# Optimization experiments

Measured on AMD Instinct MI355X. Metric: run time of the kernel, lower is better.

Reference implementation:

```python
import jax, jax.numpy as jnp
import numpy as np

B, S, E, H, A = 2, 1024, 1024, 16, 3
HD = E // H

def setup_inputs() -> dict:
    key = jax.random.key(0)
    ks = jax.random.split(key, 8)
    return {
        "query": jax.random.normal(ks[0], (B, S, E), dtype=jnp.float32),
        "key": jax.random.normal(ks[1], (B, S, E), dtype=jnp.float32),
        "value": jax.random.normal(ks[2], (B, S, E), dtype=jnp.float32),
        "aid": jax.random.normal(ks[3], (B, S, S, A), dtype=jnp.float32),
        "mixer_w": jax.random.uniform(ks[4], (H, A + 1, 1), dtype=jnp.float32),
        "mixer_b": jax.random.uniform(ks[5], (H, 1), dtype=jnp.float32),
        "Wo": jax.random.normal(ks[6], (E, E), dtype=jnp.float32) * 0.02,
        "bo": jax.random.normal(ks[7], (E,), dtype=jnp.float32) * 0.02,
        "aid_scale": jnp.array([0.1], dtype=jnp.float32),
    }

def reference(query, key, value, aid, mixer_w, mixer_b, Wo, bo, aid_scale):
    scale = HD ** -0.5
    # Faithful to source: raw row-major reshape (B,S,E)->(B,H,S,HD)
    q = query.reshape(B, H, S, HD)
    k = key.reshape(B, H, S, HD)
    v = value.reshape(B, H, S, HD)
    attn = jnp.einsum('bhqd,bhkd->bhqk', q, k) * scale  # (B,H,S,S)
    aid_h = jnp.broadcast_to(aid[:, None], (B, H, S, S, A))
    mix_in = jnp.concatenate([attn[..., None], aid_h], axis=-1)  # (B,H,S,S,A+1)
    mixed = jnp.einsum('bhqki,hio->bhqko', mix_in, mixer_w) + mixer_b[None, :, None, None, :]
    mixed = jax.nn.relu(mixed)[..., 0]  # (B,H,S,S)
    attn = attn + mixed * aid_scale[0]
    pre_softmax_attn = attn
    attn = jax.nn.softmax(attn, axis=-1)
    out = jnp.einsum('bhqk,bhkd->bhqd', attn, v)
    out = out.transpose(0, 2, 1, 3).reshape(B, S, E)
    out = out @ Wo.T + bo
    return out, attn, pre_softmax_attn
```

## Files before the change

### kernel.cpp

```cpp
#include <hip/hip_runtime.h>
#include <hip/hip_bf16.h>

using u16 = unsigned short;
typedef __attribute__((ext_vector_type(8))) short short8;
typedef __attribute__((ext_vector_type(4))) float f32x4;

constexpr int Bc = 2, Sc = 1024, Ec = 1024, Hc = 16, HDc = 64;
constexpr float SCALE = 0.125f;

__device__ __forceinline__ u16 f2bf(float f) {
    union { float f; unsigned u; } v{f};
    unsigned r = v.u + 0x7FFF + ((v.u >> 16) & 1);
    return (u16)(r >> 16);
}
__device__ __forceinline__ float bf2f(u16 x) {
    union { unsigned u; float f; } v; v.u = ((unsigned)x) << 16; return v.f;
}

__global__ __launch_bounds__(256) void k_prep(
    const float* __restrict__ Q, const float* __restrict__ K,
    const float* __restrict__ Wo, u16* __restrict__ Qb,
    u16* __restrict__ Kb, u16* __restrict__ Wob)
{
    const int bid = blockIdx.x;
    const float* src; u16* dst; int base;
    if (bid < 1024)      { src = Q;  dst = Qb;  base = bid; }
    else if (bid < 2048) { src = K;  dst = Kb;  base = bid - 1024; }
    else                 { src = Wo; dst = Wob; base = bid - 2048; }
    const int i = (base * 256 + threadIdx.x) * 8;
    float4 a = *(const float4*)&src[i];
    float4 b = *(const float4*)&src[i + 4];
    u16 t[8] = {f2bf(a.x), f2bf(a.y), f2bf(a.z), f2bf(a.w),
                f2bf(b.x), f2bf(b.y), f2bf(b.z), f2bf(b.w)};
    *(short8*)&dst[i] = *(short8*)t;
}

__global__ __launch_bounds__(256) void k_convT(const float* __restrict__ V,
                                               u16* __restrict__ Vt) {
    __shared__ float tile[64][65];
    const int bh = blockIdx.y;
    const int k0 = blockIdx.x * 64;
    const float* Vp = V + (size_t)bh * Sc * HDc + (size_t)k0 * HDc;
    const int tid = threadIdx.x;

    #pragma unroll
    for (int it = 0; it < 4; ++it) {
        int idx = tid + it * 256;
        int k = idx >> 4, d4 = idx & 15;
        float4 v = *(const float4*)&Vp[k * HDc + d4 * 4];
        tile[d4 * 4 + 0][k] = v.x;
        tile[d4 * 4 + 1][k] = v.y;
        tile[d4 * 4 + 2][k] = v.z;
        tile[d4 * 4 + 3][k] = v.w;
    }
    __syncthreads();

    u16* Op = Vt + (size_t)bh * HDc * Sc + k0;
    #pragma unroll
    for (int it = 0; it < 4; ++it) {
        int idx = tid + it * 256;
        int d = idx >> 4, kq = idx & 15;
        u16 t[4];
        #pragma unroll
        for (int j = 0; j < 4; ++j) t[j] = f2bf(tile[d][kq * 4 + j]);
        *(uint2*)&Op[(size_t)d * Sc + kq * 4] = *(uint2*)t;
    }
}

__global__ __launch_bounds__(256, 2) void k_scores(
    const u16* __restrict__ Qb, const u16* __restrict__ Kb,
    const float* __restrict__ aid, const float* __restrict__ mw,
    const float* __restrict__ mb, const float* __restrict__ ascale,
    float* __restrict__ pre)
{
    __shared__ u16 Qs[64 * 64];
    __shared__ u16 Ks[64 * 64];

    const int bid = blockIdx.x;
    const int kt = bid & 15;
    const int qt = (bid >> 4) & 15;
    const int b  = bid >> 8;

    const int tid = threadIdx.x;
    const int w = tid >> 6, lane = tid & 63;
    const int lrow = lane & 15, lhi = lane >> 4;

    float a3[4][4][3];
    #pragma unroll
    for (int r = 0; r < 4; ++r) {
        const size_t qg = (size_t)(b * Sc + qt * 64 + w * 16 + lhi * 4 + r) * Sc;
        #pragma unroll
        for (int fk = 0; fk < 4; ++fk) {
            const float* ap = aid + (qg + kt * 64 + fk * 16 + lrow) * 3;
            float2 t2 = *(const float2*)ap;
            a3[r][fk][0] = t2.x; a3[r][fk][1] = t2.y; a3[r][fk][2] = ap[2];
        }
    }

    const float asc = ascale[0];
    const u16* Qbase = Qb + ((size_t)b * Hc * Sc + qt * 64) * HDc;
    const u16* Kbase = Kb + ((size_t)b * Hc * Sc + kt * 64) * HDc;

    const int r0 = tid >> 3,          g0 = tid & 7;
    const int r1 = (tid + 256) >> 3,  g1 = tid & 7;
    const int gs0 = (g0 ^ (r0 & 7)) * 8;
    const int gs1 = (g1 ^ (r1 & 7)) * 8;

    short8 qp0, qp1, kp0, kp1;
    {
        const u16* Qp = Qbase;
        const u16* Kp = Kbase;
        qp0 = *(const short8*)&Qp[r0 * 64 + g0 * 8];
        qp1 = *(const short8*)&Qp[r1 * 64 + g1 * 8];
        kp0 = *(const short8*)&Kp[r0 * 64 + g0 * 8];
        kp1 = *(const short8*)&Kp[r1 * 64 + g1 * 8];
    }

    for (int h = 0; h < Hc; ++h) {
        *(short8*)&Qs[r0 * 64 + gs0] = qp0;
        *(short8*)&Qs[r1 * 64 + gs1] = qp1;
        *(short8*)&Ks[r0 * 64 + gs0] = kp0;
        *(short8*)&Ks[r1 * 64 + gs1] = kp1;
        __syncthreads();

        if (h < Hc - 1) {
            const u16* Qp = Qbase + (size_t)(h + 1) * Sc * HDc;
            const u16* Kp = Kbase + (size_t)(h + 1) * Sc * HDc;
            qp0 = *(const short8*)&Qp[r0 * 64 + g0 * 8];
            qp1 = *(const short8*)&Qp[r1 * 64 + g1 * 8];
            kp0 = *(const short8*)&Kp[r0 * 64 + g0 * 8];
            kp1 = *(const short8*)&Kp[r1 * 64 + g1 * 8];
        }

        f32x4 acc[4] = {};
        #pragma unroll
        for (int ks2 = 0; ks2 < 2; ++ks2) {
            const int rq = w * 16 + lrow;
            short8 af = *(const short8*)&Qs[rq * 64 + ((ks2 * 4 + lhi) ^ (rq & 7)) * 8];
            #pragma unroll
            for (int fk = 0; fk < 4; ++fk) {
                const int rk = fk * 16 + lrow;
                short8 bf = *(const short8*)&Ks[rk * 64 + ((ks2 * 4 + lhi) ^ (rk & 7)) * 8];
                acc[fk] = __builtin_amdgcn_mfma_f32_16x16x32_bf16(af, bf, acc[fk], 0, 0, 0);
            }
        }

        const float w0 = mw[h * 4 + 0], w1 = mw[h * 4 + 1];
        const float w2 = mw[h * 4 + 2], w3 = mw[h * 4 + 3];
        const float bias = mb[h];
        float* prow0 = pre + ((size_t)(b * Hc + h) * Sc + qt * 64 + w * 16 + lhi * 4) * Sc
                     + kt * 64 + lrow;
        #pragma unroll
        for (int r = 0; r < 4; ++r) {
            #pragma unroll
            for (int fk = 0; fk < 4; ++fk) {
                float s = acc[fk][r] * SCALE;
                float mm = s * w0 + a3[r][fk][0] * w1 + a3[r][fk][1] * w2
                         + a3[r][fk][2] * w3 + bias;
                prow0[(size_t)r * Sc + fk * 16] = s + fmaxf(mm, 0.f) * asc;
            }
        }
        __syncthreads();
    }
}

__global__ __launch_bounds__(512, 4) void k_spv(
    const float* __restrict__ pre, const u16* __restrict__ Vt,
    float* __restrict__ attn, u16* __restrict__ Omid)
{
    __shared__ u16 band[32 * 1024];
    __shared__ float s_m[32], s_l[32];

    const int bid = blockIdx.x;
    const int bh  = bid >> 5;
    const int qt  = (bid & 31) * 32;
    const int b   = bh >> 4, h = bh & 15;

    const int tid  = threadIdx.x;
    const int w    = tid >> 6, lane = tid & 63;
    const int lrow = lane & 15, lhi = lane >> 4;

    const int arow = tid >> 4;
    const int s16  = tid & 15;
    const int g    = s16 & 7;
    const int kh   = s16 >> 3;
    const int asw  = arow & 7;
    const float* prow = pre + ((size_t)bh * Sc + qt + arow) * Sc;
    float m = -1e30f;
    #pragma unroll
    for (int k2 = 0; k2 < 8; ++k2) {
        const int kt = kh * 8 + k2;
        const float* p0 = prow + kt * 64 + g * 8;
        float s[8];
        *(float4*)&s[0] = *(const float4*)p0;
        *(float4*)&s[4] = *(const float4*)(p0 + 4);
        u16 t[8];
        #pragma unroll
        for (int j = 0; j < 8; ++j) { m = fmaxf(m, s[j]); t[j] = f2bf(s[j]); }
        *(short8*)&band[arow * 1024 + (kt * 8 + (g ^ asw)) * 8] = *(short8*)t;
    }
    m = fmaxf(m, __shfl_xor(m, 1));
    m = fmaxf(m, __shfl_xor(m, 2));
    m = fmaxf(m, __shfl_xor(m, 4));
    m = fmaxf(m, __shfl_xor(m, 8));
    if (s16 == 0) s_m[arow] = m;
    __syncthreads();

    const int rf = w & 1, df = w >> 1;
    const int brow = rf * 16 + lrow;
    const int bsw  = brow & 7;
    const float mreg = s_m[brow];
    const u16* vrow = Vt + (size_t)bh * HDc * Sc + (size_t)(df * 16 + lrow) * Sc;
    float l = 0.f;
    f32x4 acc = {};

    #pragma unroll 4
    for (int kt = 0; kt < 16; ++kt) {
        short8 ra = *(const short8*)&band[brow * 1024 + (kt * 8 + (lhi ^ bsw)) * 8];
        short8 rb = *(const short8*)&band[brow * 1024 + (kt * 8 + ((lhi + 4) ^ bsw)) * 8];
        u16 ea[8], eb[8];
        #pragma unroll
        for (int j = 0; j < 8; ++j) {
            float va = __expf(bf2f((u16)ra[j]) - mreg); l += va; ea[j] = f2bf(va);
            float vb = __expf(bf2f((u16)rb[j]) - mreg); l += vb; eb[j] = f2bf(vb);
        }
        short8 A0 = *(short8*)ea, A1 = *(short8*)eb;
        short8 b0 = *(const short8*)&vrow[kt * 64 + lhi * 8];
        short8 b1 = *(const short8*)&vrow[kt * 64 + (lhi + 4) * 8];
        acc = __builtin_amdgcn_mfma_f32_16x16x32_bf16(A0, b0, acc, 0, 0, 0);
        acc = __builtin_amdgcn_mfma_f32_16x16x32_bf16(A1, b1, acc, 0, 0, 0);
    }
    l += __shfl_xor(l, 16);
    l += __shfl_xor(l, 32);
    if (df == 0 && lhi == 0) s_l[brow] = l;
    __syncthreads();

    const float mf  = s_m[arow];
    const float inv = 1.f / s_l[arow];
    float* arowp = attn + ((size_t)bh * Sc + qt + arow) * Sc;
    #pragma unroll
    for (int k2 = 0; k2 < 8; ++k2) {
        const int kt = kh * 8 + k2;
        short8 ra = *(const short8*)&band[arow * 1024 + (kt * 8 + (g ^ asw)) * 8];
        float o[8];
        #pragma unroll
        for (int j = 0; j < 8; ++j) o[j] = __expf(bf2f((u16)ra[j]) - mf) * inv;
        *(float4*)&arowp[kt * 64 + g * 8]     = *(float4*)&o[0];
        *(float4*)&arowp[kt * 64 + g * 8 + 4] = *(float4*)&o[4];
    }

    #pragma unroll
    for (int reg = 0; reg < 4; ++reg) {
        const int rowO = rf * 16 + lhi * 4 + reg;
        const float linv = 1.f / s_l[rowO];
        u16* orow = Omid + ((size_t)b * Sc + qt + rowO) * Ec + h * HDc;
        orow[df * 16 + lrow] = f2bf(acc[reg] * linv);
    }
}

__global__ __launch_bounds__(256, 2) void k_proj(
    const u16* __restrict__ Ob, const u16* __restrict__ Wob,
    const float* __restrict__ bo, float* __restrict__ out)
{
    __shared__ u16 Xs[128 * 64];
    __shared__ u16 Ws[64 * 64];

    const int bid = blockIdx.x;
    const int mt = (bid >> 4) * 128;
    const int et = (bid & 15) * 64;

    const int tid = threadIdx.x;
    const int w = tid >> 6, lane = tid & 63;
    const int lrow = lane & 15, lhi = lane >> 4;

    f32x4 acc[2][4] = {};

    for (int kb = 0; kb < Ec; kb += 64) {
        #pragma unroll
        for (int it = 0; it < 4; ++it) {
            int idx = tid + it * 256;
            int r = idx >> 3, g = idx & 7;
            *(short8*)&Xs[r * 64 + (g ^ (r & 7)) * 8] =
                *(const short8*)&Ob[(size_t)(mt + r) * Ec + kb + g * 8];
        }
        #pragma unroll
        for (int it = 0; it < 2; ++it) {
            int idx = tid + it * 256;
            int r = idx >> 3, g = idx & 7;
            *(short8*)&Ws[r * 64 + (g ^ (r & 7)) * 8] =
                *(const short8*)&Wob[(size_t)(et + r) * Ec + kb + g * 8];
        }
        __syncthreads();

        #pragma unroll
        for (int ks = 0; ks < 2; ++ks) {
            short8 af[2], bfr[4];
            int g = ks * 4 + lhi;
            #pragma unroll
            for (int fq = 0; fq < 2; ++fq) {
                int rq = w * 32 + fq * 16 + lrow;
                af[fq] = *(const short8*)&Xs[rq * 64 + (g ^ (rq & 7)) * 8];
            }
            #pragma unroll
            for (int fd = 0; fd < 4; ++fd) {
                int rv = fd * 16 + lrow;
                bfr[fd] = *(const short8*)&Ws[rv * 64 + (g ^ (rv & 7)) * 8];
            }
            #pragma unroll
            for (int fq = 0; fq < 2; ++fq)
                #pragma unroll
                for (int fd = 0; fd < 4; ++fd)
                    acc[fq][fd] = __builtin_amdgcn_mfma_f32_16x16x32_bf16(
                        af[fq], bfr[fd], acc[fq][fd], 0, 0, 0);
        }
        __syncthreads();
    }

    #pragma unroll
    for (int fq = 0; fq < 2; ++fq)
        #pragma unroll
        for (int r = 0; r < 4; ++r) {
            const int m = mt + w * 32 + fq * 16 + lhi * 4 + r;
            float* orow = out + (size_t)m * Ec + et;
            #pragma unroll
            for (int fd = 0; fd < 4; ++fd) {
                int e = fd * 16 + lrow;
                orow[e] = acc[fq][fd][r] + bo[et + e];
            }
        }
}

extern "C" void kernel_launch(void* const* d_in, const int* in_sizes, int n_in,
                              void* d_out, int out_size, void* d_ws, size_t ws_size,
                              hipStream_t stream) {
    const float* query  = (const float*)d_in[0];
    const float* key    = (const float*)d_in[1];
    const float* value  = (const float*)d_in[2];
    const float* aid    = (const float*)d_in[3];
    const float* mw     = (const float*)d_in[4];
    const float* mb     = (const float*)d_in[5];
    const float* Wo     = (const float*)d_in[6];
    const float* bo     = (const float*)d_in[7];
    const float* ascale = (const float*)d_in[8];

    float* out_p  = (float*)d_out;
    float* attn_p = out_p + (size_t)Bc * Sc * Ec;
    float* pre_p  = attn_p + (size_t)Bc * Hc * Sc * Sc;

    u16* Vtb  = (u16*)d_ws;
    u16* Omid = Vtb  + (size_t)2 * 1024 * 1024;
    u16* Qb   = Omid + (size_t)2 * 1024 * 1024;
    u16* Kb   = Qb   + (size_t)2 * 1024 * 1024;
    u16* Wob  = Kb   + (size_t)2 * 1024 * 1024;

    k_prep<<<2560, 256, 0, stream>>>(query, key, Wo, Qb, Kb, Wob);
    k_convT<<<dim3(Sc / 64, Bc * Hc), 256, 0, stream>>>(value, Vtb);
    k_scores<<<Bc * 16 * 16, 256, 0, stream>>>(Qb, Kb, aid, mw, mb, ascale, pre_p);
    k_spv<<<Bc * Hc * (Sc / 32), 512, 0, stream>>>(pre_p, Vtb, attn_p, Omid);
    k_proj<<<(Bc * Sc / 128) * (Ec / 64), 256, 0, stream>>>(Omid, Wob, bo, out_p);
}
```

Baseline: 144.2 us.

## Merge V transpose into prep kernel and split PV over key chunks

The V transpose moves into the prep kernel, so one launch disappears. In k_spv the eight waves now split the key dimension instead of the head dimension. Each wave computes the exponentials once for its key chunk, writes them back into the shared band, and accumulates all four d-fragments, so later passes no longer recompute exp. Partial row sums and output accumulators are reduced through shared memory, which adds syncs and LDS traffic, and attention probabilities are now derived from bf16-rounded exp values.

```diff
diff --git a/kernel.cpp b/kernel.cpp
--- a/kernel.cpp
+++ b/kernel.cpp
@@ -19,29 +19,32 @@
 
 __global__ __launch_bounds__(256) void k_prep(
     const float* __restrict__ Q, const float* __restrict__ K,
-    const float* __restrict__ Wo, u16* __restrict__ Qb,
-    u16* __restrict__ Kb, u16* __restrict__ Wob)
+    const float* __restrict__ Wo, const float* __restrict__ V,
+    u16* __restrict__ Qb, u16* __restrict__ Kb, u16* __restrict__ Wob,
+    u16* __restrict__ Vt)
 {
+    __shared__ float tile[64][65];
     const int bid = blockIdx.x;
-    const float* src; u16* dst; int base;
-    if (bid < 1024)      { src = Q;  dst = Qb;  base = bid; }
-    else if (bid < 2048) { src = K;  dst = Kb;  base = bid - 1024; }
-    else                 { src = Wo; dst = Wob; base = bid - 2048; }
-    const int i = (base * 256 + threadIdx.x) * 8;
-    float4 a = *(const float4*)&src[i];
-    float4 b = *(const float4*)&src[i + 4];
-    u16 t[8] = {f2bf(a.x), f2bf(a.y), f2bf(a.z), f2bf(a.w),
-                f2bf(b.x), f2bf(b.y), f2bf(b.z), f2bf(b.w)};
-    *(short8*)&dst[i] = *(short8*)t;
-}
-
-__global__ __launch_bounds__(256) void k_convT(const float* __restrict__ V,
-                                               u16* __restrict__ Vt) {
-    __shared__ float tile[64][65];
-    const int bh = blockIdx.y;
-    const int k0 = blockIdx.x * 64;
+    const int tid = threadIdx.x;
+
+    if (bid < 2560) {
+        const float* src; u16* dst; int base;
+        if (bid < 1024)      { src = Q;  dst = Qb;  base = bid; }
+        else if (bid < 2048) { src = K;  dst = Kb;  base = bid - 1024; }
+        else                 { src = Wo; dst = Wob; base = bid - 2048; }
+        const int i = (base * 256 + tid) * 8;
+        float4 a = *(const float4*)&src[i];
+        float4 b = *(const float4*)&src[i + 4];
+        u16 t[8] = {f2bf(a.x), f2bf(a.y), f2bf(a.z), f2bf(a.w),
+                    f2bf(b.x), f2bf(b.y), f2bf(b.z), f2bf(b.w)};
+        *(short8*)&dst[i] = *(short8*)t;
+        return;
+    }
+
+    const int bx = bid - 2560;
+    const int bh = bx >> 4;
+    const int k0 = (bx & 15) * 64;
     const float* Vp = V + (size_t)bh * Sc * HDc + (size_t)k0 * HDc;
-    const int tid = threadIdx.x;
 
     #pragma unroll
     for (int it = 0; it < 4; ++it) {
@@ -108,12 +111,10 @@
 
     short8 qp0, qp1, kp0, kp1;
     {
-        const u16* Qp = Qbase;
-        const u16* Kp = Kbase;
-        qp0 = *(const short8*)&Qp[r0 * 64 + g0 * 8];
-        qp1 = *(const short8*)&Qp[r1 * 64 + g1 * 8];
-        kp0 = *(const short8*)&Kp[r0 * 64 + g0 * 8];
-        kp1 = *(const short8*)&Kp[r1 * 64 + g1 * 8];
+        qp0 = *(const short8*)&Qbase[r0 * 64 + g0 * 8];
+        qp1 = *(const short8*)&Qbase[r1 * 64 + g1 * 8];
+        kp0 = *(const short8*)&Kbase[r0 * 64 + g0 * 8];
+        kp1 = *(const short8*)&Kbase[r1 * 64 + g1 * 8];
     }
 
     for (int h = 0; h < Hc; ++h) {
@@ -169,7 +170,8 @@
     float* __restrict__ attn, u16* __restrict__ Omid)
 {
     __shared__ u16 band[32 * 1024];
-    __shared__ float s_m[32], s_l[32];
+    __shared__ float s_m[32];
+    __shared__ float s_lp[4][32];
 
     const int bid = blockIdx.x;
     const int bh  = bid >> 5;
@@ -206,37 +208,46 @@
     if (s16 == 0) s_m[arow] = m;
     __syncthreads();
 
-    const int rf = w & 1, df = w >> 1;
+    const int rf = w & 1, kf = w >> 1;
     const int brow = rf * 16 + lrow;
     const int bsw  = brow & 7;
     const float mreg = s_m[brow];
-    const u16* vrow = Vt + (size_t)bh * HDc * Sc + (size_t)(df * 16 + lrow) * Sc;
+    const u16* Vbase = Vt + (size_t)bh * HDc * Sc;
     float l = 0.f;
-    f32x4 acc = {};
-
-    #pragma unroll 4
-    for (int kt = 0; kt < 16; ++kt) {
-        short8 ra = *(const short8*)&band[brow * 1024 + (kt * 8 + (lhi ^ bsw)) * 8];
-        short8 rb = *(const short8*)&band[brow * 1024 + (kt * 8 + ((lhi + 4) ^ bsw)) * 8];
+    f32x4 acc[4] = {};
+
+    #pragma unroll
+    for (int j = 0; j < 4; ++j) {
+        const int kt = kf * 4 + j;
+        const int soA = brow * 1024 + (kt * 8 + (lhi ^ bsw)) * 8;
+        const int soB = brow * 1024 + (kt * 8 + ((lhi + 4) ^ bsw)) * 8;
+        short8 ra = *(const short8*)&band[soA];
+        short8 rb = *(const short8*)&band[soB];
         u16 ea[8], eb[8];
         #pragma unroll
-        for (int j = 0; j < 8; ++j) {
-            float va = __expf(bf2f((u16)ra[j]) - mreg); l += va; ea[j] = f2bf(va);
-            float vb = __expf(bf2f((u16)rb[j]) - mreg); l += vb; eb[j] = f2bf(vb);
-        }
+        for (int jj = 0; jj < 8; ++jj) {
+            float va = __expf(bf2f((u16)ra[jj]) - mreg); l += va; ea[jj] = f2bf(va);
+            float vb = __expf(bf2f((u16)rb[jj]) - mreg); l += vb; eb[jj] = f2bf(vb);
+        }
+        *(short8*)&band[soA] = *(short8*)ea;
+        *(short8*)&band[soB] = *(short8*)eb;
         short8 A0 = *(short8*)ea, A1 = *(short8*)eb;
-        short8 b0 = *(const short8*)&vrow[kt * 64 + lhi * 8];
-        short8 b1 = *(const short8*)&vrow[kt * 64 + (lhi + 4) * 8];
-        acc = __builtin_amdgcn_mfma_f32_16x16x32_bf16(A0, b0, acc, 0, 0, 0);
-        acc = __builtin_amdgcn_mfma_f32_16x16x32_bf16(A1, b1, acc, 0, 0, 0);
+        #pragma unroll
+        for (int fd = 0; fd < 4; ++fd) {
+            const u16* vp = Vbase + (size_t)(fd * 16 + lrow) * Sc + kt * 64;
+            short8 b0 = *(const short8*)&vp[lhi * 8];
+            short8 b1 = *(const short8*)&vp[(lhi + 4) * 8];
+            acc[fd] = __builtin_amdgcn_mfma_f32_16x16x32_bf16(A0, b0, acc[fd], 0, 0, 0);
+            acc[fd] = __builtin_amdgcn_mfma_f32_16x16x32_bf16(A1, b1, acc[fd], 0, 0, 0);
+        }
     }
     l += __shfl_xor(l, 16);
     l += __shfl_xor(l, 32);
-    if (df == 0 && lhi == 0) s_l[brow] = l;
-    __syncthreads();
-
-    const float mf  = s_m[arow];
-    const float inv = 1.f / s_l[arow];
+    if (lhi == 0) s_lp[kf][brow] = l;
+    __syncthreads();
+
+    const float lt = s_lp[0][arow] + s_lp[1][arow] + s_lp[2][arow] + s_lp[3][arow];
+    const float inv = 1.f / lt;
     float* arowp = attn + ((size_t)bh * Sc + qt + arow) * Sc;
     #pragma unroll
     for (int k2 = 0; k2 < 8; ++k2) {
@@ -244,18 +255,35 @@
         short8 ra = *(const short8*)&band[arow * 1024 + (kt * 8 + (g ^ asw)) * 8];
         float o[8];
         #pragma unroll
-        for (int j = 0; j < 8; ++j) o[j] = __expf(bf2f((u16)ra[j]) - mf) * inv;
+        for (int jj = 0; jj < 8; ++jj) o[jj] = bf2f((u16)ra[jj]) * inv;
         *(float4*)&arowp[kt * 64 + g * 8]     = *(float4*)&o[0];
         *(float4*)&arowp[kt * 64 + g * 8 + 4] = *(float4*)&o[4];
     }
-
+    __syncthreads();
+
+    float* ovl = (float*)band;
     #pragma unroll
     for (int reg = 0; reg < 4; ++reg) {
         const int rowO = rf * 16 + lhi * 4 + reg;
-        const float linv = 1.f / s_l[rowO];
-        u16* orow = Omid + ((size_t)b * Sc + qt + rowO) * Ec + h * HDc;
-        orow[df * 16 + lrow] = f2bf(acc[reg] * linv);
-    }
+        #pragma unroll
+        for (int fd = 0; fd < 4; ++fd)
+            ovl[(kf * 32 + rowO) * 68 + fd * 16 + lrow] = acc[fd][reg];
+    }
+    __syncthreads();
+
+    const int orow_ = tid >> 4;
+    const int dq    = tid & 15;
+    const float lr = 1.f / (s_lp[0][orow_] + s_lp[1][orow_]
+                          + s_lp[2][orow_] + s_lp[3][orow_]);
+    u16 t4[4];
+    #pragma unroll
+    for (int dd = 0; dd < 4; ++dd) {
+        const int d = dq * 4 + dd;
+        float v = ovl[(0 * 32 + orow_) * 68 + d] + ovl[(1 * 32 + orow_) * 68 + d]
+                + ovl[(2 * 32 + orow_) * 68 + d] + ovl[(3 * 32 + orow_) * 68 + d];
+        t4[dd] = f2bf(v * lr);
+    }
+    *(uint2*)&Omid[((size_t)b * Sc + qt + orow_) * Ec + h * HDc + dq * 4] = *(uint2*)t4;
 }
 
 __global__ __launch_bounds__(256, 2) void k_proj(
@@ -353,8 +381,7 @@
     u16* Kb   = Qb   + (size_t)2 * 1024 * 1024;
     u16* Wob  = Kb   + (size_t)2 * 1024 * 1024;
 
-    k_prep<<<2560, 256, 0, stream>>>(query, key, Wo, Qb, Kb, Wob);
-    k_convT<<<dim3(Sc / 64, Bc * Hc), 256, 0, stream>>>(value, Vtb);
+    k_prep<<<3072, 256, 0, stream>>>(query, key, Wo, value, Qb, Kb, Wob, Vtb);
     k_scores<<<Bc * 16 * 16, 256, 0, stream>>>(Qb, Kb, aid, mw, mb, ascale, pre_p);
     k_spv<<<Bc * Hc * (Sc / 32), 512, 0, stream>>>(pre_p, Vtb, attn_p, Omid);
     k_proj<<<(Bc * Sc / 128) * (Ec / 64), 256, 0, stream>>>(Omid, Wob, bo, out_p);
```

After: 141.9 us. Within noise of the previous version (-1.6%).
